# Performance work log

Hardware: AMD Instinct MI355X
Metric: run time of the kernel (lower is better)

## Reference

```python
import jax, jax.numpy as jnp
import numpy as np

B, T, C = 2, 2048, 1024
N_HEADS = 16
HEAD_DIM = C // N_HEADS

def setup_inputs() -> dict:
    key = jax.random.key(0)
    k1, k2, k3 = jax.random.split(key, 3)
    x = jax.random.normal(k1, (B, T, C), dtype=jnp.float32)
    W_qkv = jax.random.normal(k2, (C, 3 * C), dtype=jnp.float32) * (1.0 / np.sqrt(C))
    W_out = jax.random.normal(k3, (C, C), dtype=jnp.float32) * (1.0 / np.sqrt(C))
    return {"x": x, "W_qkv": W_qkv, "W_out": W_out}

def reference(x, W_qkv, W_out):
    b, t, c = x.shape
    qkv = jnp.einsum('btc,cd->btd', x, W_qkv)  # [B,T,3C]
    q, k, v = jnp.split(qkv, 3, axis=-1)
    # [B, H, T, hd]
    q = q.reshape(b, t, N_HEADS, HEAD_DIM).transpose(0, 2, 1, 3)
    k = k.reshape(b, t, N_HEADS, HEAD_DIM).transpose(0, 2, 1, 3)
    v = v.reshape(b, t, N_HEADS, HEAD_DIM).transpose(0, 2, 1, 3)
    scale = 1.0 / jnp.sqrt(jnp.asarray(HEAD_DIM, dtype=x.dtype))
    attn = jnp.einsum('bhqd,bhkd->bhqk', q, k) * scale  # [B,H,T,T]
    causal = jnp.tril(jnp.ones((t, t), dtype=bool))
    attn = jnp.where(causal, attn, jnp.asarray(-1e9, dtype=attn.dtype))
    attn = jax.nn.softmax(attn, axis=-1)
    out = jnp.einsum('bhqk,bhkd->bhqd', attn, v)
    out = out.transpose(0, 2, 1, 3).reshape(b, t, c)
    return jnp.einsum('btc,cd->btd', out, W_out)
```

## Files before the change

### kernel.cpp

```cpp
#include <hip/hip_runtime.h>
#include <hip/hip_bf16.h>

typedef __attribute__((ext_vector_type(8))) short short8;
typedef __attribute__((ext_vector_type(4))) short bf16x4;
typedef __attribute__((ext_vector_type(4))) float floatx4;

#define T_SEQ 2048
#define NH    16
#define HD    64
#define QSCALE 0.18033688f

#define MFMA16(a, b, c) __builtin_amdgcn_mfma_f32_16x16x16bf16_1k(a, b, c, 0, 0, 0)
#define MFMA32(a, b, c) __builtin_amdgcn_mfma_f32_16x16x32_bf16(a, b, c, 0, 0, 0)

__device__ __forceinline__ ushort f2bf(float f) {
    union { float f; unsigned u; } un; un.f = f;
    unsigned r = un.u + 0x7fff + ((un.u >> 16) & 1);
    return (ushort)(r >> 16);
}
__device__ __forceinline__ unsigned pkbf(float a, float b) {
    __hip_bfloat162 t = __float22bfloat162_rn(float2{a, b});
    return *reinterpret_cast<unsigned*>(&t);
}

typedef const __attribute__((address_space(1))) unsigned int* gp1_t;
typedef __attribute__((address_space(3))) unsigned int* lp3_t;
__device__ __forceinline__ void gl_lds16(const ushort* g, ushort* l) {
    __builtin_amdgcn_global_load_lds((gp1_t)g, (lp3_t)l, 16, 0, 0);
}

__global__ void prep_kernel(const float* __restrict__ Wqkv, const float* __restrict__ Wout,
                            const float* __restrict__ x, ushort* __restrict__ wt_qkv,
                            ushort* __restrict__ wt_out, ushort* __restrict__ x_bf) {
    __shared__ ushort tile[32][33];
    const int bid = blockIdx.x;
    if (bid >= 4096) {
        size_t i = ((size_t)(bid - 4096) * 256 + threadIdx.x) * 8;
        float4 f0 = *(const float4*)(x + i);
        float4 f1 = *(const float4*)(x + i + 4);
        short8 v;
        v[0] = (short)f2bf(f0.x); v[1] = (short)f2bf(f0.y);
        v[2] = (short)f2bf(f0.z); v[3] = (short)f2bf(f0.w);
        v[4] = (short)f2bf(f1.x); v[5] = (short)f2bf(f1.y);
        v[6] = (short)f2bf(f1.z); v[7] = (short)f2bf(f1.w);
        *(short8*)(x_bf + i) = v;
        return;
    }
    const float* in; ushort* out; int R, C, gx, gy;
    if (bid < 3072) { in = Wqkv; out = wt_qkv; R = 1024; C = 3072; gx = bid % 96; gy = bid / 96; }
    else            { int t = bid - 3072; in = Wout; out = wt_out; R = 1024; C = 1024; gx = t & 31; gy = t >> 5; }
    const int tx = threadIdx.x & 31, ty = threadIdx.x >> 5;
    const int bx = gx * 32, by = gy * 32;
    #pragma unroll
    for (int i = ty; i < 32; i += 8)
        tile[i][tx] = f2bf(in[(size_t)(by + i) * C + bx + tx]);
    __syncthreads();
    #pragma unroll
    for (int i = ty; i < 32; i += 8)
        out[(size_t)(bx + i) * R + by + tx] = tile[tx][i];
}

template <int EPI>
__global__ __launch_bounds__(256, 2)
void gemm_bt(const ushort* __restrict__ A, const ushort* __restrict__ Bt,
             void* __restrict__ O0, ushort* __restrict__ O1, ushort* __restrict__ O2,
             int M, int N, int K) {
    __shared__ __align__(16) ushort smem[16384];
    ushort* As = smem;
    ushort* Bs = smem + 8192;
    const int tid  = threadIdx.x;
    const int wave = tid >> 6, lane = tid & 63;
    const int quad = lane >> 4, l16 = lane & 15;
    const int wm = (wave >> 1) * 64, wn = (wave & 1) * 64;

    const int nwg = gridDim.x * gridDim.y;
    const int lid = blockIdx.y * gridDim.x + blockIdx.x;
    const int cpx = nwg >> 3;
    const int swz = (lid & 7) * cpx + (lid >> 3);
    const int m0 = (swz / gridDim.y) * 128;
    const int n0 = (swz % gridDim.y) * 128;

    const ushort* aP[4];
    const ushort* bP[4];
    #pragma unroll
    for (int j = 0; j < 4; j++) {
        int c = tid + j * 256;
        int r = c >> 3;
        int g = ((c & 7) ^ (r & 7)) * 8;
        aP[j] = A  + (size_t)(m0 + r) * K + g;
        bP[j] = Bt + (size_t)(n0 + r) * K + g;
    }

    floatx4 acc[4][4];
    #pragma unroll
    for (int i = 0; i < 4; i++)
        #pragma unroll
        for (int j = 0; j < 4; j++)
            acc[i][j] = (floatx4){0.f, 0.f, 0.f, 0.f};

    const int xsw = l16 & 7;

    for (int k0 = 0; k0 < K; k0 += 64) {
        __syncthreads();
        #pragma unroll
        for (int j = 0; j < 4; j++) gl_lds16(aP[j] + k0, &As[(tid + j * 256) * 8]);
        #pragma unroll
        for (int j = 0; j < 4; j++) gl_lds16(bP[j] + k0, &Bs[(tid + j * 256) * 8]);
        __syncthreads();
        #pragma unroll
        for (int kk = 0; kk < 2; kk++) {
            short8 af[4], bf[4];
            #pragma unroll
            for (int i = 0; i < 4; i++)
                af[i] = *(const short8*)(&As[(wm + i * 16 + l16) * 64 + ((kk * 4 + quad) ^ xsw) * 8]);
            #pragma unroll
            for (int j = 0; j < 4; j++)
                bf[j] = *(const short8*)(&Bs[(wn + j * 16 + l16) * 64 + ((kk * 4 + quad) ^ xsw) * 8]);
            #pragma unroll
            for (int i = 0; i < 4; i++)
                #pragma unroll
                for (int j = 0; j < 4; j++)
                    acc[i][j] = MFMA32(af[i], bf[j], acc[i][j]);
        }
    }

    if (EPI == 0 && n0 >= 2048) {
        const int b = m0 >> 11;
        const int t0 = m0 & 2047;
        const int head0 = (n0 - 2048) >> 6;
        __syncthreads();
        #pragma unroll
        for (int nh = 0; nh < 2; nh++) {
            if ((wave & 1) == nh) {
                #pragma unroll
                for (int j = 0; j < 4; j++)
                    #pragma unroll
                    for (int i = 0; i < 4; i++) {
                        int nl = j * 16 + l16;
                        int mB = wm + i * 16 + quad * 4;
                        *(unsigned*)(&smem[nl * 136 + mB])     = pkbf(acc[i][j][0], acc[i][j][1]);
                        *(unsigned*)(&smem[nl * 136 + mB + 2]) = pkbf(acc[i][j][2], acc[i][j][3]);
                    }
            }
            __syncthreads();
            #pragma unroll
            for (int cc = 0; cc < 4; cc++) {
                int c = cc * 256 + tid;
                int row = c >> 4, mcol = (c & 15) * 8;
                uint4 v = *(const uint4*)(&smem[row * 136 + mcol]);
                *(uint4*)(&O2[((size_t)(b * NH + head0 + nh) * HD + row) * T_SEQ + t0 + mcol]) = v;
            }
            __syncthreads();
        }
        return;
    }

    #pragma unroll
    for (int i = 0; i < 4; i++) {
        #pragma unroll
        for (int j = 0; j < 4; j++) {
            #pragma unroll
            for (int r = 0; r < 4; r++) {
                int m = m0 + wm + i * 16 + quad * 4 + r;
                int n = n0 + wn + j * 16 + l16;
                if (EPI == 0) {
                    int b = m >> 11, t = m & 2047;
                    int part = n >> 10, c = n & 1023;
                    int head = c >> 6, off = c & 63;
                    float av = acc[i][j][r];
                    if (part == 0) av *= QSCALE;
                    ushort v = f2bf(av);
                    if (part == 0) ((ushort*)O0)[(((size_t)(b * NH + head)) * T_SEQ + t) * HD + off] = v;
                    else           O1[(((size_t)(b * NH + head)) * T_SEQ + t) * HD + off] = v;
                } else {
                    ((float*)O0)[(size_t)m * N + n] = acc[i][j][r];
                }
            }
        }
    }
}

__device__ __forceinline__ void softmax_step(floatx4 s[4], float& mst, float& ll,
                                             floatx4 o[4], bf16x4 pf[4]) {
    float t0 = fmaxf(fmaxf(s[0][0], s[0][1]), fmaxf(s[0][2], s[0][3]));
    float t1 = fmaxf(fmaxf(s[1][0], s[1][1]), fmaxf(s[1][2], s[1][3]));
    float t2 = fmaxf(fmaxf(s[2][0], s[2][1]), fmaxf(s[2][2], s[2][3]));
    float t3 = fmaxf(fmaxf(s[3][0], s[3][1]), fmaxf(s[3][2], s[3][3]));
    float t  = fmaxf(fmaxf(t0, t1), fmaxf(t2, t3));
    if (!__all(t - mst <= 8.0f)) {
        t = fmaxf(t, __shfl_xor(t, 16));
        t = fmaxf(t, __shfl_xor(t, 32));
        float mnew  = fmaxf(mst, t);
        float alpha = exp2f(mst - mnew);
        mst = mnew;
        ll  *= alpha;
        #pragma unroll
        for (int db = 0; db < 4; db++)
            #pragma unroll
            for (int r = 0; r < 4; r++) o[db][r] *= alpha;
    }
    #pragma unroll
    for (int j = 0; j < 4; j++) {
        float p0 = exp2f(s[j][0] - mst);
        float p1 = exp2f(s[j][1] - mst);
        float p2 = exp2f(s[j][2] - mst);
        float p3 = exp2f(s[j][3] - mst);
        ll += (p0 + p1) + (p2 + p3);
        union { bf16x4 v; unsigned u[2]; } pu;
        pu.u[0] = pkbf(p0, p1);
        pu.u[1] = pkbf(p2, p3);
        pf[j] = pu.v;
    }
}

__global__ __launch_bounds__(256, 2)
void attn_kernel(const ushort* __restrict__ Q, const ushort* __restrict__ Kk,
                 const ushort* __restrict__ Vt, ushort* __restrict__ Oout) {
    __shared__ __align__(16) ushort Ks[2][128 * 64];
    __shared__ __align__(16) ushort Vs[2][64 * 128];
    const int tid  = threadIdx.x;
    const int wave = tid >> 6, lane = tid & 63;
    const int quad = lane >> 4, l16 = lane & 15;
    const int idx = blockIdx.x;
    const int bh = idx & 31;
    const int jp = idx >> 5;
    const int p  = (jp < 8) ? jp : (15 - (jp - 8));
    const int qtA = p, qtB = 31 - p;
    const int b = bh >> 4, h = bh & 15;

    const ushort* qp = Q  + (size_t)bh * T_SEQ * HD;
    const ushort* kp = Kk + (size_t)bh * T_SEQ * HD;
    const ushort* vp = Vt + (size_t)bh * HD * T_SEQ;

    const int q0A = qtA * 64 + wave * 16;
    const int q0B = qtB * 64 + wave * 16;

    short8 qfA[2], qfB[2];
    #pragma unroll
    for (int kb = 0; kb < 2; kb++) {
        qfA[kb] = *(const short8*)(qp + (size_t)(q0A + l16) * HD + kb * 32 + quad * 8);
        qfB[kb] = *(const short8*)(qp + (size_t)(q0B + l16) * HD + kb * 32 + quad * 8);
    }

    floatx4 oA[4], oB[4];
    #pragma unroll
    for (int db = 0; db < 4; db++) {
        oA[db] = (floatx4){0.f, 0.f, 0.f, 0.f};
        oB[db] = (floatx4){0.f, 0.f, 0.f, 0.f};
    }
    float mA = -1e30f, llA = 0.f, mB = -1e30f, llB = 0.f;

    int koff[4], voff[4];
    #pragma unroll
    for (int j = 0; j < 4; j++) {
        int c = tid + j * 256;
        int kr = c >> 3;
        koff[j] = kr * HD + (((c & 7) ^ (kr & 7)) * 8);
        int vr = c >> 4;
        voff[j] = vr * T_SEQ + ((((c & 15) ^ (vr & 7))) * 8);
    }

#define STAGE(BUF, I)                                                            \
    {                                                                            \
        const ushort* kg = kp + (size_t)(I) * 128 * HD;                          \
        const ushort* vg = vp + (I) * 128;                                       \
        gl_lds16(kg + koff[0], &Ks[BUF][(tid      ) * 8]);                       \
        gl_lds16(kg + koff[1], &Ks[BUF][(tid + 256) * 8]);                       \
        gl_lds16(kg + koff[2], &Ks[BUF][(tid + 512) * 8]);                       \
        gl_lds16(kg + koff[3], &Ks[BUF][(tid + 768) * 8]);                       \
        gl_lds16(vg + voff[0], &Vs[BUF][(tid      ) * 8]);                       \
        gl_lds16(vg + voff[1], &Vs[BUF][(tid + 256) * 8]);                       \
        gl_lds16(vg + voff[2], &Vs[BUF][(tid + 512) * 8]);                       \
        gl_lds16(vg + voff[3], &Vs[BUF][(tid + 768) * 8]);                       \
    }

    const int xsw = (l16 & 7), qh = quad >> 1, ql = quad & 1;
    const int ka0 = l16 * 64 + ((quad ^ xsw) * 8);
    const int ka1 = l16 * 64 + (((4 + quad) ^ xsw) * 8);
    int va[4];
    #pragma unroll
    for (int jj = 0; jj < 4; jj++)
        va[jj] = l16 * 128 + (((2 * jj + qh) ^ xsw) * 8) + ql * 4;

#define ZS(S) { _Pragma("unroll") for (int z = 0; z < 4; z++) S[z] = (floatx4){0.f, 0.f, 0.f, 0.f}; }

#define QKD(SB, SA, BUF, ST)                                                     \
    {                                                                            \
        _Pragma("unroll")                                                        \
        for (int jj = 0; jj < 4; jj++) {                                         \
            short8 kf = *(const short8*)(&Ks[BUF][(ST) * 4096 + jj * 1024 + ka0]); \
            SB[jj] = MFMA32(kf, qfB[0], SB[jj]);                                 \
            SA[jj] = MFMA32(kf, qfA[0], SA[jj]);                                 \
        }                                                                        \
        _Pragma("unroll")                                                        \
        for (int jj = 0; jj < 4; jj++) {                                         \
            short8 kf = *(const short8*)(&Ks[BUF][(ST) * 4096 + jj * 1024 + ka1]); \
            SB[jj] = MFMA32(kf, qfB[1], SB[jj]);                                 \
            SA[jj] = MFMA32(kf, qfA[1], SA[jj]);                                 \
        }                                                                        \
    }

#define QK1(SB, BUF, ST)                                                         \
    {                                                                            \
        _Pragma("unroll")                                                        \
        for (int jj = 0; jj < 4; jj++) {                                         \
            short8 kf = *(const short8*)(&Ks[BUF][(ST) * 4096 + jj * 1024 + ka0]); \
            SB[jj] = MFMA32(kf, qfB[0], SB[jj]);                                 \
        }                                                                        \
        _Pragma("unroll")                                                        \
        for (int jj = 0; jj < 4; jj++) {                                         \
            short8 kf = *(const short8*)(&Ks[BUF][(ST) * 4096 + jj * 1024 + ka1]); \
            SB[jj] = MFMA32(kf, qfB[1], SB[jj]);                                 \
        }                                                                        \
    }

#define MASKD(S)                                                                 \
    {                                                                            \
        _Pragma("unroll")                                                        \
        for (int jj = 0; jj < 4; jj++)                                           \
            _Pragma("unroll")                                                    \
            for (int rr = 0; rr < 4; rr++)                                       \
                if (jj * 16 + quad * 4 + rr > wave * 16 + l16) S[jj][rr] = -1e30f; \
    }

#define PVG(O, PF, BUF, ST)                                                      \
    {                                                                            \
        _Pragma("unroll")                                                        \
        for (int jj = 0; jj < 4; jj++)                                           \
            _Pragma("unroll")                                                    \
            for (int db = 0; db < 4; db++) {                                     \
                bf16x4 vf = *(const bf16x4*)(&Vs[BUF][va[jj] + (ST) * 64 + db * 2048]); \
                O[db] = MFMA16(vf, PF[jj], O[db]);                               \
            }                                                                    \
    }

#define ITER(BUF, I)                                                             \
    {                                                                            \
        __syncthreads();                                                         \
        if ((I) + 1 < NT) STAGE((BUF) ^ 1, (I) + 1)                              \
        const int kt0 = 2 * (I), kt1 = kt0 + 1;                                  \
        const bool v1 = (kt1 <= qtB);                                            \
        const bool a0 = (kt0 <= qtA), a1 = (kt1 <= qtA);                         \
        floatx4 sB0[4], sB1[4], sA0[4], sA1[4];                                  \
        bf16x4 pfB0[4], pfB1[4], pfA0[4], pfA1[4];                               \
        __builtin_amdgcn_s_setprio(1);                                           \
        ZS(sB0)                                                                  \
        if (a0) { ZS(sA0) QKD(sB0, sA0, BUF, 0) } else { QK1(sB0, BUF, 0) }      \
        if (v1) {                                                                \
            ZS(sB1)                                                              \
            if (a1) { ZS(sA1) QKD(sB1, sA1, BUF, 1) } else { QK1(sB1, BUF, 1) }  \
        }                                                                        \
        __builtin_amdgcn_s_setprio(0);                                           \
        if (kt0 == qtB) { MASKD(sB0) }                                           \
        if (v1 && kt1 == qtB) { MASKD(sB1) }                                     \
        if (a0 && kt0 == qtA) { MASKD(sA0) }                                     \
        if (a1 && kt1 == qtA) { MASKD(sA1) }                                     \
        softmax_step(sB0, mB, llB, oB, pfB0);                                    \
        PVG(oB, pfB0, BUF, 0)                                                    \
        if (v1) { softmax_step(sB1, mB, llB, oB, pfB1); PVG(oB, pfB1, BUF, 1) }  \
        if (a0) { softmax_step(sA0, mA, llA, oA, pfA0); PVG(oA, pfA0, BUF, 0) }  \
        if (a1) { softmax_step(sA1, mA, llA, oA, pfA1); PVG(oA, pfA1, BUF, 1) }  \
    }

    const int NT = (qtB + 2) >> 1;
    STAGE(0, 0)

    int i = 0;
    for (; i + 1 < NT; i += 2) {
        ITER(0, i)
        ITER(1, i + 1)
    }
    if (i < NT) ITER(0, i)
#undef ITER
#undef PVG
#undef MASKD
#undef QK1
#undef QKD
#undef ZS
#undef STAGE

    {
        float lB = llB;
        lB += __shfl_xor(lB, 16);
        lB += __shfl_xor(lB, 32);
        const float inv = 1.0f / lB;
        const int t = q0B + l16;
        #pragma unroll
        for (int db = 0; db < 4; db++) {
            union { ushort4 w; unsigned u[2]; } ou;
            ou.u[0] = pkbf(oB[db][0] * inv, oB[db][1] * inv);
            ou.u[1] = pkbf(oB[db][2] * inv, oB[db][3] * inv);
            *(ushort4*)(Oout + (((size_t)b * T_SEQ + t) * NH + h) * HD + db * 16 + quad * 4) = ou.w;
        }
    }
    {
        float lA = llA;
        lA += __shfl_xor(lA, 16);
        lA += __shfl_xor(lA, 32);
        const float inv = 1.0f / lA;
        const int t = q0A + l16;
        #pragma unroll
        for (int db = 0; db < 4; db++) {
            union { ushort4 w; unsigned u[2]; } ou;
            ou.u[0] = pkbf(oA[db][0] * inv, oA[db][1] * inv);
            ou.u[1] = pkbf(oA[db][2] * inv, oA[db][3] * inv);
            *(ushort4*)(Oout + (((size_t)b * T_SEQ + t) * NH + h) * HD + db * 16 + quad * 4) = ou.w;
        }
    }
}

extern "C" void kernel_launch(void* const* d_in, const int* in_sizes, int n_in,
                              void* d_out, int out_size, void* d_ws, size_t ws_size,
                              hipStream_t stream) {
    const float* x    = (const float*)d_in[0];
    const float* Wqkv = (const float*)d_in[1];
    const float* Wout = (const float*)d_in[2];
    ushort* ws = (ushort*)d_ws;

    ushort* wt_qkv = ws;
    ushort* wt_out = wt_qkv + 3072 * 1024;
    ushort* q_ws   = wt_out + 1024 * 1024;
    ushort* k_ws   = q_ws + 4194304;
    ushort* v_t    = k_ws + 4194304;
    ushort* a_out  = v_t + 4194304;
    ushort* x_bf   = a_out + 4194304;

    prep_kernel<<<dim3(6144), 256, 0, stream>>>(Wqkv, Wout, x, wt_qkv, wt_out, x_bf);

    gemm_bt<0><<<dim3(32, 24), 256, 0, stream>>>(x_bf, wt_qkv, q_ws, k_ws, v_t, 4096, 3072, 1024);

    attn_kernel<<<dim3(512), 256, 0, stream>>>(q_ws, k_ws, v_t, a_out);

    gemm_bt<1><<<dim3(32, 8), 256, 0, stream>>>(a_out, wt_out, (float*)d_out, nullptr, nullptr,
                                                4096, 1024, 1024);
}
```

Before: 176.9 us.

## Stage Q/K epilogue through LDS and use narrower N tile for output GEMM

The QKV GEMM epilogue for Q and K now writes bf16 values into a padded LDS tile and then stores 16-byte rows to global memory, replacing scattered 2-byte stores. The GEMM is templated on the N tile width, and the output projection now uses a 64-wide tile with twice as many workgroups. The narrower tile is meant to fill more compute units on the small output GEMM. The cost is lower per-block data reuse and extra barriers in the epilogue.

```diff
diff --git a/kernel.cpp b/kernel.cpp
--- a/kernel.cpp
+++ b/kernel.cpp
@@ -60,42 +60,50 @@
         out[(size_t)(bx + i) * R + by + tx] = tile[tx][i];
 }
 
-template <int EPI>
+template <int EPI, int BN>
 __global__ __launch_bounds__(256, 2)
 void gemm_bt(const ushort* __restrict__ A, const ushort* __restrict__ Bt,
              void* __restrict__ O0, ushort* __restrict__ O1, ushort* __restrict__ O2,
              int M, int N, int K) {
-    __shared__ __align__(16) ushort smem[16384];
+    constexpr int NJ = BN / 32;
+    constexpr int NB = (BN * 8) / 256;
+    __shared__ __align__(16) ushort smem[8192 + BN * 64];
     ushort* As = smem;
     ushort* Bs = smem + 8192;
     const int tid  = threadIdx.x;
     const int wave = tid >> 6, lane = tid & 63;
     const int quad = lane >> 4, l16 = lane & 15;
-    const int wm = (wave >> 1) * 64, wn = (wave & 1) * 64;
+    const int wm = (wave >> 1) * 64, wn = (wave & 1) * (BN / 2);
 
     const int nwg = gridDim.x * gridDim.y;
     const int lid = blockIdx.y * gridDim.x + blockIdx.x;
     const int cpx = nwg >> 3;
     const int swz = (lid & 7) * cpx + (lid >> 3);
     const int m0 = (swz / gridDim.y) * 128;
-    const int n0 = (swz % gridDim.y) * 128;
+    const int n0 = (swz % gridDim.y) * BN;
 
     const ushort* aP[4];
-    const ushort* bP[4];
+    const ushort* bP[NB];
     #pragma unroll
     for (int j = 0; j < 4; j++) {
         int c = tid + j * 256;
         int r = c >> 3;
         int g = ((c & 7) ^ (r & 7)) * 8;
-        aP[j] = A  + (size_t)(m0 + r) * K + g;
+        aP[j] = A + (size_t)(m0 + r) * K + g;
+    }
+    #pragma unroll
+    for (int j = 0; j < NB; j++) {
+        int c = tid + j * 256;
+        int r = c >> 3;
+        int g = ((c & 7) ^ (r & 7)) * 8;
         bP[j] = Bt + (size_t)(n0 + r) * K + g;
     }
 
-    floatx4 acc[4][4];
+    floatx4 acc[4][NJ];
     #pragma unroll
     for (int i = 0; i < 4; i++)
         #pragma unroll
-        for (int j = 0; j < 4; j++)
+        for (int j = 0; j < NJ; j++)
             acc[i][j] = (floatx4){0.f, 0.f, 0.f, 0.f};
 
     const int xsw = l16 & 7;
@@ -103,80 +111,101 @@
     for (int k0 = 0; k0 < K; k0 += 64) {
         __syncthreads();
         #pragma unroll
-        for (int j = 0; j < 4; j++) gl_lds16(aP[j] + k0, &As[(tid + j * 256) * 8]);
-        #pragma unroll
-        for (int j = 0; j < 4; j++) gl_lds16(bP[j] + k0, &Bs[(tid + j * 256) * 8]);
+        for (int j = 0; j < 4; j++)  gl_lds16(aP[j] + k0, &As[(tid + j * 256) * 8]);
+        #pragma unroll
+        for (int j = 0; j < NB; j++) gl_lds16(bP[j] + k0, &Bs[(tid + j * 256) * 8]);
         __syncthreads();
         #pragma unroll
         for (int kk = 0; kk < 2; kk++) {
-            short8 af[4], bf[4];
+            short8 af[4], bf[NJ];
             #pragma unroll
             for (int i = 0; i < 4; i++)
                 af[i] = *(const short8*)(&As[(wm + i * 16 + l16) * 64 + ((kk * 4 + quad) ^ xsw) * 8]);
             #pragma unroll
-            for (int j = 0; j < 4; j++)
+            for (int j = 0; j < NJ; j++)
                 bf[j] = *(const short8*)(&Bs[(wn + j * 16 + l16) * 64 + ((kk * 4 + quad) ^ xsw) * 8]);
             #pragma unroll
             for (int i = 0; i < 4; i++)
                 #pragma unroll
-                for (int j = 0; j < 4; j++)
+                for (int j = 0; j < NJ; j++)
                     acc[i][j] = MFMA32(af[i], bf[j], acc[i][j]);
         }
     }
 
-    if (EPI == 0 && n0 >= 2048) {
+    if constexpr (EPI == 0) {
         const int b = m0 >> 11;
         const int t0 = m0 & 2047;
-        const int head0 = (n0 - 2048) >> 6;
-        __syncthreads();
-        #pragma unroll
-        for (int nh = 0; nh < 2; nh++) {
-            if ((wave & 1) == nh) {
+        if (n0 >= 2048) {
+            const int head0 = (n0 - 2048) >> 6;
+            __syncthreads();
+            #pragma unroll
+            for (int nh = 0; nh < 2; nh++) {
+                if ((wave & 1) == nh) {
+                    #pragma unroll
+                    for (int j = 0; j < NJ; j++)
+                        #pragma unroll
+                        for (int i = 0; i < 4; i++) {
+                            int nl = j * 16 + l16;
+                            int mB = wm + i * 16 + quad * 4;
+                            *(unsigned*)(&smem[nl * 136 + mB])     = pkbf(acc[i][j][0], acc[i][j][1]);
+                            *(unsigned*)(&smem[nl * 136 + mB + 2]) = pkbf(acc[i][j][2], acc[i][j][3]);
+                        }
+                }
+                __syncthreads();
                 #pragma unroll
-                for (int j = 0; j < 4; j++)
+                for (int cc = 0; cc < 4; cc++) {
+                    int c = cc * 256 + tid;
+                    int row = c >> 4, mcol = (c & 15) * 8;
+                    uint4 v = *(const uint4*)(&smem[row * 136 + mcol]);
+                    *(uint4*)(&O2[((size_t)(b * NH + head0 + nh) * HD + row) * T_SEQ + t0 + mcol]) = v;
+                }
+                __syncthreads();
+            }
+        } else {
+            __syncthreads();
+            #pragma unroll
+            for (int nh = 0; nh < 2; nh++) {
+                const int nn = n0 + nh * 64;
+                const int part = nn >> 10;
+                const int head = (nn & 1023) >> 6;
+                ushort* OP = (part == 0) ? (ushort*)O0 : O1;
+                const float qs = (part == 0) ? QSCALE : 1.0f;
+                if ((wave & 1) == nh) {
                     #pragma unroll
-                    for (int i = 0; i < 4; i++) {
-                        int nl = j * 16 + l16;
-                        int mB = wm + i * 16 + quad * 4;
-                        *(unsigned*)(&smem[nl * 136 + mB])     = pkbf(acc[i][j][0], acc[i][j][1]);
-                        *(unsigned*)(&smem[nl * 136 + mB + 2]) = pkbf(acc[i][j][2], acc[i][j][3]);
-                    }
+                    for (int i = 0; i < 4; i++)
+                        #pragma unroll
+                        for (int j = 0; j < NJ; j++) {
+                            const int col = j * 16 + l16;
+                            const int rowb = wm + i * 16 + quad * 4;
+                            #pragma unroll
+                            for (int r = 0; r < 4; r++)
+                                smem[(rowb + r) * 72 + col] = f2bf(acc[i][j][r] * qs);
+                        }
+                }
+                __syncthreads();
+                const size_t obase = ((size_t)(b * NH + head)) * T_SEQ + t0;
+                #pragma unroll
+                for (int cc = 0; cc < 4; cc++) {
+                    int c = cc * 256 + tid;
+                    int row = c >> 3, col8 = (c & 7) * 8;
+                    uint4 v = *(const uint4*)(&smem[row * 72 + col8]);
+                    *(uint4*)(&OP[(obase + row) * HD + col8]) = v;
+                }
+                __syncthreads();
             }
-            __syncthreads();
-            #pragma unroll
-            for (int cc = 0; cc < 4; cc++) {
-                int c = cc * 256 + tid;
-                int row = c >> 4, mcol = (c & 15) * 8;
-                uint4 v = *(const uint4*)(&smem[row * 136 + mcol]);
-                *(uint4*)(&O2[((size_t)(b * NH + head0 + nh) * HD + row) * T_SEQ + t0 + mcol]) = v;
-            }
-            __syncthreads();
         }
         return;
-    }
-
-    #pragma unroll
-    for (int i = 0; i < 4; i++) {
-        #pragma unroll
-        for (int j = 0; j < 4; j++) {
-            #pragma unroll
-            for (int r = 0; r < 4; r++) {
-                int m = m0 + wm + i * 16 + quad * 4 + r;
-                int n = n0 + wn + j * 16 + l16;
-                if (EPI == 0) {
-                    int b = m >> 11, t = m & 2047;
-                    int part = n >> 10, c = n & 1023;
-                    int head = c >> 6, off = c & 63;
-                    float av = acc[i][j][r];
-                    if (part == 0) av *= QSCALE;
-                    ushort v = f2bf(av);
-                    if (part == 0) ((ushort*)O0)[(((size_t)(b * NH + head)) * T_SEQ + t) * HD + off] = v;
-                    else           O1[(((size_t)(b * NH + head)) * T_SEQ + t) * HD + off] = v;
-                } else {
+    } else {
+        #pragma unroll
+        for (int i = 0; i < 4; i++)
+            #pragma unroll
+            for (int j = 0; j < NJ; j++)
+                #pragma unroll
+                for (int r = 0; r < 4; r++) {
+                    int m = m0 + wm + i * 16 + quad * 4 + r;
+                    int n = n0 + wn + j * 16 + l16;
                     ((float*)O0)[(size_t)m * N + n] = acc[i][j][r];
                 }
-            }
-        }
     }
 }
 
@@ -427,10 +456,11 @@
 
     prep_kernel<<<dim3(6144), 256, 0, stream>>>(Wqkv, Wout, x, wt_qkv, wt_out, x_bf);
 
-    gemm_bt<0><<<dim3(32, 24), 256, 0, stream>>>(x_bf, wt_qkv, q_ws, k_ws, v_t, 4096, 3072, 1024);
+    gemm_bt<0, 128><<<dim3(32, 24), 256, 0, stream>>>(x_bf, wt_qkv, q_ws, k_ws, v_t,
+                                                      4096, 3072, 1024);
 
     attn_kernel<<<dim3(512), 256, 0, stream>>>(q_ws, k_ws, v_t, a_out);
 
-    gemm_bt<1><<<dim3(32, 8), 256, 0, stream>>>(a_out, wt_out, (float*)d_out, nullptr, nullptr,
-                                                4096, 1024, 1024);
-}
+    gemm_bt<1, 64><<<dim3(32, 16), 256, 0, stream>>>(a_out, wt_out, (float*)d_out, nullptr, nullptr,
+                                                     4096, 1024, 1024);
+}
```

Result: no change. 177.1 us (+0.1%).
